# Performance work log

Measured on AMD Instinct MI355X. Metric: run time of the kernel, lower is better.

Reference implementation:

```python
import jax, jax.numpy as jnp
import numpy as np


def setup_inputs() -> dict:
    key = jax.random.key(0)
    k1, k2, k3 = jax.random.split(key, 3)
    b, n, h, d = 2, 2048, 16, 64
    q = jax.random.normal(k1, (b, n, h, d), dtype=jnp.float32)
    k = jax.random.normal(k2, (b, n, h, d), dtype=jnp.float32)
    v = jax.random.normal(k3, (b, n, h, d), dtype=jnp.float32)
    return {"q": q, "k": k, "v": v, "is_causal": 1}


def reference(q, k, v, is_causal):
    # q, k, v: [b, n, h, d]
    b, n, h, d = q.shape
    scale = 1.0 / jnp.sqrt(jnp.asarray(d, dtype=q.dtype))
    # scores: [b, h, n_q, n_k]
    scores = jnp.einsum("bqhd,bkhd->bhqk", q, k) * scale
    if is_causal:
        causal_mask = jnp.triu(jnp.ones((n, n), dtype=bool), k=1)  # True above diagonal
        scores = jnp.where(causal_mask[None, None, :, :], jnp.asarray(-jnp.inf, scores.dtype), scores)
    attn = jax.nn.softmax(scores, axis=-1)
    # output back to [b, n, h, d]
    out = jnp.einsum("bhqk,bkhd->bqhd", attn, v)
    return out
```

## Files before the change

### kernel.cpp

```cpp
#include <hip/hip_runtime.h>
#include <hip/hip_bf16.h>
#include <math.h>

typedef __bf16 bf16x8 __attribute__((ext_vector_type(8)));
typedef __bf16 bf16x4 __attribute__((ext_vector_type(4)));
typedef __bf16 bf16x2 __attribute__((ext_vector_type(2)));
typedef float  f32x4  __attribute__((ext_vector_type(4)));
typedef float  f32x16 __attribute__((ext_vector_type(16)));
typedef unsigned int u32;
typedef unsigned int u32x4 __attribute__((ext_vector_type(4)));

#define HD   64
#define NQB  16
#define MNEG (-1e30f)
#define KSW(r, c) ((c) ^ (((r) & 7) << 3))
#define VSW(r, c) ((c) ^ ((((r) >> 2) & 7) << 3))

static __device__ __forceinline__ u32 pkbf(float a, float b) {
  bf16x2 t; t[0] = (__bf16)a; t[1] = (__bf16)b;
  return __builtin_bit_cast(u32, t);
}

__global__ __launch_bounds__(256, 2)
void fattn_fwd(const float* __restrict__ Q, const float* __restrict__ K,
               const float* __restrict__ V, const int* __restrict__ causal_p,
               float* __restrict__ O, int B, int N, int H) {
  __shared__ alignas(16) __bf16 Kl[64][64];
  __shared__ alignas(16) __bf16 Vt[64][64];

  const int tid  = threadIdx.x;
  const int wave = tid >> 6;
  const int lane = tid & 63;
  const int l31  = lane & 31;
  const int h    = lane >> 5;
  const int lo16 = lane & 15, hi4 = lane >> 4;

  const int x  = (NQB - 1) - ((int)blockIdx.x >> 5);
  const int bh = blockIdx.x & 31;
  const int bb = bh / H, hh = bh - bb * H;

  const int causal = causal_p[0];
  const int sN = H * HD;

  const float* Qb = Q + (long)bb * N * sN + hh * HD;
  const float* Kb = K + (long)bb * N * sN + hh * HD;
  const float* Vb = V + (long)bb * N * sN + hh * HD;
  float*       Ob = O + (long)bb * N * sN + hh * HD;

  const int q0w   = x * 128 + wave * 32;
  const int ntile = causal ? (2 * x + 2) : (2 * NQB);

  const float qscale = 0.125f * 1.44269504088896340736f;
  bf16x8 aq[4];
  {
    const float* qrow = Qb + (long)(q0w + l31) * sN;
#pragma unroll
    for (int ds = 0; ds < 4; ++ds) {
      f32x4 x0 = *(const f32x4*)(qrow + ds * 16 + h * 8);
      f32x4 x1 = *(const f32x4*)(qrow + ds * 16 + h * 8 + 4);
      bf16x8 a;
#pragma unroll
      for (int j = 0; j < 4; ++j) {
        a[j]     = (__bf16)(x0[j] * qscale);
        a[j + 4] = (__bf16)(x1[j] * qscale);
      }
      aq[ds] = a;
    }
  }

  f32x16 accA, accB;
#pragma unroll
  for (int j = 0; j < 16; ++j) { accA[j] = 0.f; accB[j] = 0.f; }
  float m_run = MNEG, l_run = 0.f;

  f32x4 kreg[4], vreg[4];
  auto issue = [&](int tt) {
    const int k0 = tt * 64;
#pragma unroll
    for (int i = 0; i < 4; ++i) {
      const int fl = tid + i * 256;
      const int r = fl >> 4, c4 = (fl & 15) * 4;
      kreg[i] = *(const f32x4*)(Kb + (long)(k0 + r) * sN + c4);
    }
    const float* vrow = Vb + (long)(k0 + wave * 16 + hi4 * 4) * sN + lo16 * 4;
#pragma unroll
    for (int q = 0; q < 4; ++q) vreg[q] = *(const f32x4*)(vrow + (long)q * sN);
  };
  auto wr = [&]() {
#pragma unroll
    for (int i = 0; i < 4; ++i) {
      const int fl = tid + i * 256;
      const int r = fl >> 4, c4 = (fl & 15) * 4;
      bf16x4 kb;
#pragma unroll
      for (int j = 0; j < 4; ++j) kb[j] = (__bf16)kreg[i][j];
      *(bf16x4*)&Kl[r][KSW(r, c4)] = kb;
    }
    const int kv0 = wave * 16 + hi4 * 4;
#pragma unroll
    for (int j = 0; j < 4; ++j) {
      const int d = lo16 * 4 + j;
      bf16x4 vv;
#pragma unroll
      for (int q = 0; q < 4; ++q) vv[q] = (__bf16)vreg[q][j];
      *(bf16x4*)&Vt[d][VSW(d, kv0)] = vv;
    }
  };

  issue(0);
  wr();
  __syncthreads();

  for (int t = 0; t < ntile; ++t) {
    const bool pf = (t + 1 < ntile);
    if (pf) issue(t + 1);
    const int k0 = t * 64;

    f32x16 p0, p1;
#pragma unroll
    for (int j = 0; j < 16; ++j) { p0[j] = 0.f; p1[j] = 0.f; }
#pragma unroll
    for (int ds = 0; ds < 4; ++ds) {
      const int cc = ds * 16 + h * 8;
      bf16x8 ka = *(const bf16x8*)&Kl[l31][KSW(l31, cc)];
      p0 = __builtin_amdgcn_mfma_f32_32x32x16_bf16(ka, aq[ds], p0, 0, 0, 0);
      bf16x8 kb2 = *(const bf16x8*)&Kl[32 + l31][KSW(32 + l31, cc)];
      p1 = __builtin_amdgcn_mfma_f32_32x32x16_bf16(kb2, aq[ds], p1, 0, 0, 0);
    }

    if (causal && t >= ntile - 2) {
      const int qg = q0w + l31;
#pragma unroll
      for (int reg = 0; reg < 16; ++reg) {
        const int crow = (reg & 3) + 8 * (reg >> 2) + 4 * h;
        if (k0 + crow > qg)      p0[reg] = MNEG;
        if (k0 + 32 + crow > qg) p1[reg] = MNEG;
      }
    }

    float t8[8];
#pragma unroll
    for (int j = 0; j < 8; ++j)
      t8[j] = fmaxf(fmaxf(p0[j], p0[j + 8]), fmaxf(p1[j], p1[j + 8]));
#pragma unroll
    for (int stp = 4; stp > 0; stp >>= 1)
#pragma unroll
      for (int j = 0; j < stp; ++j) t8[j] = fmaxf(t8[j], t8[j + stp]);
    const float mx = fmaxf(t8[0], __shfl_xor(t8[0], 32));
    const float mnew = fmaxf(m_run, mx);
    const float fac  = exp2f(m_run - mnew);
#pragma unroll
    for (int j = 0; j < 16; ++j) {
      p0[j] = exp2f(p0[j] - mnew);
      p1[j] = exp2f(p1[j] - mnew);
    }
    float s8[8];
#pragma unroll
    for (int j = 0; j < 8; ++j)
      s8[j] = (p0[j] + p0[j + 8]) + (p1[j] + p1[j + 8]);
#pragma unroll
    for (int stp = 4; stp > 0; stp >>= 1)
#pragma unroll
      for (int j = 0; j < stp; ++j) s8[j] += s8[j + stp];
    const float ps = s8[0] + __shfl_xor(s8[0], 32);
    l_run = l_run * fac + ps;
    m_run = mnew;
#pragma unroll
    for (int j = 0; j < 16; ++j) { accA[j] *= fac; accB[j] *= fac; }

    u32 W0[8], W1[8];
#pragma unroll
    for (int tt = 0; tt < 8; ++tt) {
      W0[tt] = pkbf(p0[2 * tt], p0[2 * tt + 1]);
      W1[tt] = pkbf(p1[2 * tt], p1[2 * tt + 1]);
    }
    auto mkpair = [&](u32 wa, u32 wb, u32& dlo, u32& dhi) {
      const u32 gsel = h ? wa : wb;
      const u32 f = (u32)__shfl_xor((int)gsel, 32);
      dlo = h ? f : wa;
      dhi = h ? wb : f;
    };
    bf16x8 pa[4];
    {
      u32 d0, d1, d2, d3;
      mkpair(W0[0], W0[2], d0, d2); mkpair(W0[1], W0[3], d1, d3);
      pa[0] = __builtin_bit_cast(bf16x8, (u32x4){d0, d1, d2, d3});
      mkpair(W0[4], W0[6], d0, d2); mkpair(W0[5], W0[7], d1, d3);
      pa[1] = __builtin_bit_cast(bf16x8, (u32x4){d0, d1, d2, d3});
      mkpair(W1[0], W1[2], d0, d2); mkpair(W1[1], W1[3], d1, d3);
      pa[2] = __builtin_bit_cast(bf16x8, (u32x4){d0, d1, d2, d3});
      mkpair(W1[4], W1[6], d0, d2); mkpair(W1[5], W1[7], d1, d3);
      pa[3] = __builtin_bit_cast(bf16x8, (u32x4){d0, d1, d2, d3});
    }

#pragma unroll
    for (int ks = 0; ks < 4; ++ks) {
      bf16x8 va = *(const bf16x8*)&Vt[l31][VSW(l31, ks * 16 + h * 8)];
      accA = __builtin_amdgcn_mfma_f32_32x32x16_bf16(va, pa[ks], accA, 0, 0, 0);
    }
#pragma unroll
    for (int ks = 0; ks < 4; ++ks) {
      bf16x8 va = *(const bf16x8*)&Vt[32 + l31][VSW(32 + l31, ks * 16 + h * 8)];
      accB = __builtin_amdgcn_mfma_f32_32x32x16_bf16(va, pa[ks], accB, 0, 0, 0);
    }

    __syncthreads();
    if (pf) wr();
    __syncthreads();
  }

  {
    const float linv = 1.0f / l_run;
    float* orow = Ob + (long)(q0w + l31) * sN;
#pragma unroll
    for (int g = 0; g < 4; ++g) {
      f32x4 o0, o1;
#pragma unroll
      for (int j = 0; j < 4; ++j) {
        o0[j] = accA[4 * g + j] * linv;
        o1[j] = accB[4 * g + j] * linv;
      }
      *(f32x4*)(orow + 8 * g + 4 * h) = o0;
      *(f32x4*)(orow + 32 + 8 * g + 4 * h) = o1;
    }
  }
}

extern "C" void kernel_launch(void* const* d_in, const int* in_sizes, int n_in,
                              void* d_out, int out_size, void* d_ws, size_t ws_size,
                              hipStream_t stream) {
  const float* q = (const float*)d_in[0];
  const float* k = (const float*)d_in[1];
  const float* v = (const float*)d_in[2];
  const int* causal = (const int*)d_in[3];
  float* out = (float*)d_out;
  const int B = 2, N = 2048, H = 16;
  dim3 grid(NQB * B * H);
  fattn_fwd<<<grid, dim3(256), 0, stream>>>(q, k, v, causal, out, B, N, H);
}
```

Measured before the change: 142.6 us.

## Split KV range across two blocks with merge kernel, double-buffer LDS, lazy rescale

Each query block's KV loop is split into two halves processed by separate workgroups (split-K flash attention), with partial accumulators, max and sum written to workspace and combined by a second merge kernel. This balances the causal triangle's work across more blocks. K/V LDS tiles are double-buffered so one barrier per iteration is removed. The online-softmax rescale is skipped when the max rises by no more than 8 (log2 units) across the wave. The cost is workspace traffic, an extra kernel launch, and a wider exponent range before rescaling. The split path only runs if the workspace is large enough.

```diff
diff --git a/kernel.cpp b/kernel.cpp
--- a/kernel.cpp
+++ b/kernel.cpp
@@ -11,22 +11,28 @@
 typedef unsigned int u32x4 __attribute__((ext_vector_type(4)));
 
 #define HD   64
-#define NQB  16
 #define MNEG (-1e30f)
 #define KSW(r, c) ((c) ^ (((r) & 7) << 3))
 #define VSW(r, c) ((c) ^ ((((r) >> 2) & 7) << 3))
+
+#define NSLOT   1024
+#define ACC_FL  (NSLOT * 8192)
+#define ML_FL   (NSLOT * 256)
+#define WS_NEED ((size_t)(ACC_FL + ML_FL) * 4)
 
 static __device__ __forceinline__ u32 pkbf(float a, float b) {
   bf16x2 t; t[0] = (__bf16)a; t[1] = (__bf16)b;
   return __builtin_bit_cast(u32, t);
 }
 
+template <int SPLIT>
 __global__ __launch_bounds__(256, 2)
 void fattn_fwd(const float* __restrict__ Q, const float* __restrict__ K,
                const float* __restrict__ V, const int* __restrict__ causal_p,
-               float* __restrict__ O, int B, int N, int H) {
-  __shared__ alignas(16) __bf16 Kl[64][64];
-  __shared__ alignas(16) __bf16 Vt[64][64];
+               float* __restrict__ O, float* __restrict__ wsAcc,
+               float* __restrict__ wsML, int B, int N, int H) {
+  __shared__ alignas(16) __bf16 Kl[2][64][64];
+  __shared__ alignas(16) __bf16 Vt[2][64][64];
 
   const int tid  = threadIdx.x;
   const int wave = tid >> 6;
@@ -35,11 +41,26 @@
   const int h    = lane >> 5;
   const int lo16 = lane & 15, hi4 = lane >> 4;
 
-  const int x  = (NQB - 1) - ((int)blockIdx.x >> 5);
-  const int bh = blockIdx.x & 31;
+  const int causal = causal_p[0];
+
+  int x, bh, t0, t1, slot = 0;
+  if constexpr (SPLIT) {
+    bh = (int)blockIdx.x & 31;
+    const int xc = (int)blockIdx.x >> 5;
+    x = 15 - (xc >> 1);
+    const int c = xc & 1;
+    const int ntile = causal ? (2 * x + 2) : 32;
+    t0 = c * 16;
+    t1 = min(t0 + 16, ntile);
+    if (t0 >= t1) return;
+    slot = (bh * 16 + x) * 2 + c;
+  } else {
+    x  = 15 - ((int)blockIdx.x >> 5);
+    bh = (int)blockIdx.x & 31;
+    t0 = 0;
+    t1 = causal ? (2 * x + 2) : 32;
+  }
   const int bb = bh / H, hh = bh - bb * H;
-
-  const int causal = causal_p[0];
   const int sN = H * HD;
 
   const float* Qb = Q + (long)bb * N * sN + hh * HD;
@@ -47,8 +68,7 @@
   const float* Vb = V + (long)bb * N * sN + hh * HD;
   float*       Ob = O + (long)bb * N * sN + hh * HD;
 
-  const int q0w   = x * 128 + wave * 32;
-  const int ntile = causal ? (2 * x + 2) : (2 * NQB);
+  const int q0w = x * 128 + wave * 32;
 
   const float qscale = 0.125f * 1.44269504088896340736f;
   bf16x8 aq[4];
@@ -86,7 +106,7 @@
 #pragma unroll
     for (int q = 0; q < 4; ++q) vreg[q] = *(const f32x4*)(vrow + (long)q * sN);
   };
-  auto wr = [&]() {
+  auto wr = [&](int buf) {
 #pragma unroll
     for (int i = 0; i < 4; ++i) {
       const int fl = tid + i * 256;
@@ -94,7 +114,7 @@
       bf16x4 kb;
 #pragma unroll
       for (int j = 0; j < 4; ++j) kb[j] = (__bf16)kreg[i][j];
-      *(bf16x4*)&Kl[r][KSW(r, c4)] = kb;
+      *(bf16x4*)&Kl[buf][r][KSW(r, c4)] = kb;
     }
     const int kv0 = wave * 16 + hi4 * 4;
 #pragma unroll
@@ -103,16 +123,17 @@
       bf16x4 vv;
 #pragma unroll
       for (int q = 0; q < 4; ++q) vv[q] = (__bf16)vreg[q][j];
-      *(bf16x4*)&Vt[d][VSW(d, kv0)] = vv;
+      *(bf16x4*)&Vt[buf][d][VSW(d, kv0)] = vv;
     }
   };
 
-  issue(0);
-  wr();
+  issue(t0);
+  wr(0);
   __syncthreads();
 
-  for (int t = 0; t < ntile; ++t) {
-    const bool pf = (t + 1 < ntile);
+  int pb = 0;
+  for (int t = t0; t < t1; ++t) {
+    const bool pf = (t + 1 < t1);
     if (pf) issue(t + 1);
     const int k0 = t * 64;
 
@@ -122,13 +143,13 @@
 #pragma unroll
     for (int ds = 0; ds < 4; ++ds) {
       const int cc = ds * 16 + h * 8;
-      bf16x8 ka = *(const bf16x8*)&Kl[l31][KSW(l31, cc)];
+      bf16x8 ka = *(const bf16x8*)&Kl[pb][l31][KSW(l31, cc)];
       p0 = __builtin_amdgcn_mfma_f32_32x32x16_bf16(ka, aq[ds], p0, 0, 0, 0);
-      bf16x8 kb2 = *(const bf16x8*)&Kl[32 + l31][KSW(32 + l31, cc)];
+      bf16x8 kb2 = *(const bf16x8*)&Kl[pb][32 + l31][KSW(32 + l31, cc)];
       p1 = __builtin_amdgcn_mfma_f32_32x32x16_bf16(kb2, aq[ds], p1, 0, 0, 0);
     }
 
-    if (causal && t >= ntile - 2) {
+    if (causal && t >= 2 * x) {
       const int qg = q0w + l31;
 #pragma unroll
       for (int reg = 0; reg < 16; ++reg) {
@@ -147,12 +168,18 @@
 #pragma unroll
       for (int j = 0; j < stp; ++j) t8[j] = fmaxf(t8[j], t8[j + stp]);
     const float mx = fmaxf(t8[0], __shfl_xor(t8[0], 32));
-    const float mnew = fmaxf(m_run, mx);
-    const float fac  = exp2f(m_run - mnew);
+    if (!__all(mx - m_run <= 8.0f)) {
+      const float mnew = fmaxf(m_run, mx);
+      const float fac  = exp2f(m_run - mnew);
+      l_run *= fac;
+      m_run = mnew;
+#pragma unroll
+      for (int j = 0; j < 16; ++j) { accA[j] *= fac; accB[j] *= fac; }
+    }
 #pragma unroll
     for (int j = 0; j < 16; ++j) {
-      p0[j] = exp2f(p0[j] - mnew);
-      p1[j] = exp2f(p1[j] - mnew);
+      p0[j] = exp2f(p0[j] - m_run);
+      p1[j] = exp2f(p1[j] - m_run);
     }
     float s8[8];
 #pragma unroll
@@ -163,10 +190,7 @@
 #pragma unroll
       for (int j = 0; j < stp; ++j) s8[j] += s8[j + stp];
     const float ps = s8[0] + __shfl_xor(s8[0], 32);
-    l_run = l_run * fac + ps;
-    m_run = mnew;
-#pragma unroll
-    for (int j = 0; j < 16; ++j) { accA[j] *= fac; accB[j] *= fac; }
+    l_run += ps;
 
     u32 W0[8], W1[8];
 #pragma unroll
@@ -195,21 +219,36 @@
 
 #pragma unroll
     for (int ks = 0; ks < 4; ++ks) {
-      bf16x8 va = *(const bf16x8*)&Vt[l31][VSW(l31, ks * 16 + h * 8)];
+      bf16x8 va = *(const bf16x8*)&Vt[pb][l31][VSW(l31, ks * 16 + h * 8)];
       accA = __builtin_amdgcn_mfma_f32_32x32x16_bf16(va, pa[ks], accA, 0, 0, 0);
     }
 #pragma unroll
     for (int ks = 0; ks < 4; ++ks) {
-      bf16x8 va = *(const bf16x8*)&Vt[32 + l31][VSW(32 + l31, ks * 16 + h * 8)];
+      bf16x8 va = *(const bf16x8*)&Vt[pb][32 + l31][VSW(32 + l31, ks * 16 + h * 8)];
       accB = __builtin_amdgcn_mfma_f32_32x32x16_bf16(va, pa[ks], accB, 0, 0, 0);
     }
 
+    if (pf) wr(pb ^ 1);
     __syncthreads();
-    if (pf) wr();
-    __syncthreads();
-  }
-
-  {
+    pb ^= 1;
+  }
+
+  const int qrel = wave * 32 + l31;
+  if constexpr (SPLIT) {
+    float* ap = wsAcc + (long)slot * 8192 + qrel * 64;
+#pragma unroll
+    for (int g = 0; g < 4; ++g) {
+      f32x4 o0, o1;
+#pragma unroll
+      for (int j = 0; j < 4; ++j) { o0[j] = accA[4 * g + j]; o1[j] = accB[4 * g + j]; }
+      *(f32x4*)(ap + 8 * g + 4 * h) = o0;
+      *(f32x4*)(ap + 32 + 8 * g + 4 * h) = o1;
+    }
+    if (h == 0) {
+      wsML[slot * 256 + qrel] = m_run;
+      wsML[slot * 256 + 128 + qrel] = l_run;
+    }
+  } else {
     const float linv = 1.0f / l_run;
     float* orow = Ob + (long)(q0w + l31) * sN;
 #pragma unroll
@@ -223,6 +262,49 @@
       *(f32x4*)(orow + 8 * g + 4 * h) = o0;
       *(f32x4*)(orow + 32 + 8 * g + 4 * h) = o1;
     }
+  }
+}
+
+__global__ __launch_bounds__(256)
+void fmerge(const float* __restrict__ wsAcc, const float* __restrict__ wsML,
+            const int* __restrict__ causal_p, float* __restrict__ O,
+            int B, int N, int H) {
+  const int tid = threadIdx.x;
+  const int bh = (int)blockIdx.x >> 4;
+  const int x  = (int)blockIdx.x & 15;
+  const int bb = bh / H, hh = bh - bb * H;
+  const int causal = causal_p[0];
+  const int ntile = causal ? (2 * x + 2) : 32;
+  const int q  = tid >> 1;
+  const int dh = (tid & 1) * 32;
+  const int slot0 = (bh * 16 + x) * 2;
+  const bool v1 = (16 < ntile);
+
+  const float m0 = wsML[slot0 * 256 + q];
+  const float l0 = wsML[slot0 * 256 + 128 + q];
+  const float m1 = v1 ? wsML[(slot0 + 1) * 256 + q] : MNEG;
+  const float l1 = v1 ? wsML[(slot0 + 1) * 256 + 128 + q] : 0.f;
+  const float M  = fmaxf(m0, m1);
+  const float e0 = exp2f(m0 - M);
+  const float e1 = v1 ? exp2f(m1 - M) : 0.f;
+  const float inv = 1.0f / (e0 * l0 + e1 * l1);
+  const float f0 = e0 * inv, f1 = e1 * inv;
+
+  const float* a0 = wsAcc + (long)slot0 * 8192 + q * 64 + dh;
+  const float* a1 = a0 + 8192;
+  float* op = O + ((long)(bb * N + x * 128 + q) * H + hh) * HD + dh;
+#pragma unroll
+  for (int j = 0; j < 8; ++j) {
+    f32x4 r0 = *(const f32x4*)(a0 + 4 * j);
+    f32x4 o;
+#pragma unroll
+    for (int e = 0; e < 4; ++e) o[e] = r0[e] * f0;
+    if (v1) {
+      f32x4 r1 = *(const f32x4*)(a1 + 4 * j);
+#pragma unroll
+      for (int e = 0; e < 4; ++e) o[e] += r1[e] * f1;
+    }
+    *(f32x4*)(op + 4 * j) = o;
   }
 }
 
@@ -235,6 +317,14 @@
   const int* causal = (const int*)d_in[3];
   float* out = (float*)d_out;
   const int B = 2, N = 2048, H = 16;
-  dim3 grid(NQB * B * H);
-  fattn_fwd<<<grid, dim3(256), 0, stream>>>(q, k, v, causal, out, B, N, H);
+  if (ws_size >= WS_NEED) {
+    float* wsAcc = (float*)d_ws;
+    float* wsML  = wsAcc + ACC_FL;
+    fattn_fwd<1><<<dim3(NSLOT), dim3(256), 0, stream>>>(q, k, v, causal, out,
+                                                        wsAcc, wsML, B, N, H);
+    fmerge<<<dim3(512), dim3(256), 0, stream>>>(wsAcc, wsML, causal, out, B, N, H);
+  } else {
+    fattn_fwd<0><<<dim3(512), dim3(256), 0, stream>>>(q, k, v, causal, out,
+                                                      nullptr, nullptr, B, N, H);
+  }
 }
```

New measurement: 162.2 us. 13.7% more time.
